# Performance work log

Measured on AMD Instinct MI355X. Metric: run time of the kernel, lower is better.

## Reference

```python
import jax, jax.numpy as jnp
import numpy as np

B, L, SIZE, HEADS, AH, NBR, KER, DEPTH = 64, 512, 128, 8, 16, 15, 16, 3
MAXD = 20.0
N = B * L
EDGE = KER + 3 + 9 + 1  # 29


def _normalize(v):
    return v / (jnp.linalg.norm(v, axis=-1, keepdims=True) + 1e-8)


def _frames(pos):
    # local orientation frame per residue from consecutive CA displacements
    u = _normalize(pos[1:] - pos[:-1])            # (N-1,3)
    up = jnp.concatenate([u[:1], u], axis=0)      # u_{i-1}
    un = jnp.concatenate([u, u[-1:]], axis=0)     # u_i
    b = _normalize(up - un)
    n = _normalize(jnp.cross(up, un))
    return jnp.stack([b, n, jnp.cross(b, n)], axis=-1)  # (N,3,3)


def setup_inputs() -> dict:
    key = jax.random.key(0)
    ks = jax.random.split(key, 16)
    g = lambda i, shape, s=1.0: jax.random.normal(ks[i], shape, jnp.float32) * s
    return {
        "tertiary": g(0, (N, 3, 3), 10.0),
        "sequence": g(1, (N, 20)),
        "subgraph_indices": jnp.arange(N, dtype=jnp.int32) // L,
        "knn_noise": g(2, (B, L, L)),
        "embed_w": g(3, (27, SIZE), 0.1), "embed_b": jnp.zeros((SIZE,), jnp.float32),
        "wq": g(4, (DEPTH, SIZE, HEADS * AH), 0.08),
        "wk": g(5, (DEPTH, SIZE + EDGE, HEADS * AH), 0.08),
        "wv": g(6, (DEPTH, SIZE + EDGE, HEADS * AH), 0.08),
        "wo": g(7, (DEPTH, HEADS * AH, SIZE), 0.08),
        "mlp_w1": g(8, (DEPTH, SIZE, SIZE), 0.08), "mlp_b1": jnp.zeros((DEPTH, SIZE), jnp.float32),
        "mlp_w2": g(9, (DEPTH, SIZE, SIZE), 0.08), "mlp_b2": jnp.zeros((DEPTH, SIZE), jnp.float32),
        "mlp_w3": g(10, (DEPTH, SIZE, SIZE), 0.08), "mlp_b3": jnp.zeros((DEPTH, SIZE), jnp.float32),
        "pool_w": g(11, (4, SIZE, SIZE, 3), 0.05), "pool_b": jnp.zeros((4, SIZE), jnp.float32),
        "energy_w": g(12, (SIZE, 1), 0.1), "energy_b": jnp.zeros((1,), jnp.float32),
    }


def _forward(tertiary, sequence, knn_noise, embed_w, embed_b, wq, wk, wv, wo,
             mlp_w1, mlp_b1, mlp_w2, mlp_b2, mlp_w3, mlp_b3,
             pool_w, pool_b, energy_w, energy_b):
    pos = tertiary[:, 1]                                   # (N,3) CA positions
    R = _frames(pos)                                       # (N,3,3)
    # ---- kNN per contiguous protein group with noisy distances ----
    pg = pos.reshape(B, L, 3)
    dist = jnp.linalg.norm(pg[:, :, None] - pg[:, None, :], axis=-1)  # (B,L,L)
    closeness = -dist + 3.0 * knn_noise
    idx = jax.lax.top_k(closeness, NBR)[1]                 # (B,L,NBR) local
    nbr = (idx + (jnp.arange(B) * L)[:, None, None]).reshape(N, NBR)
    # ---- RBF relative encoding (RelativeStructure.message) ----
    dvec = pos[nbr] - pos[:, None]                         # (N,NBR,3)
    d = jnp.linalg.norm(dvec, axis=-1)                     # (N,NBR)
    mu = jnp.linspace(0.0, MAXD, KER)
    sigma = MAXD / KER
    rbf = jnp.exp(-(((d[..., None] - mu) / sigma) ** 2))   # (N,NBR,KER)
    dirs = jnp.einsum('nrc,nkr->nkc', R, dvec / (d[..., None] + 1e-8))
    relrot = jnp.einsum('nrc,nkrd->nkcd', R, R[nbr]).reshape(N, NBR, 9)
    ind = jnp.arange(N, dtype=tertiary.dtype)
    relind = (ind[nbr] - ind[:, None])[..., None]
    edge = jnp.concatenate([rbf, dirs, relrot, relind], axis=-1)  # (N,NBR,EDGE)
    # ---- structured graph-attention encoder ----
    h = jnp.ones((N, 27), tertiary.dtype) @ embed_w + embed_b
    inv_sqrt = 1.0 / np.sqrt(AH).astype(np.float32)
    for l in range(DEPTH):
        q = (h @ wq[l]).reshape(N, HEADS, AH)
        kv = jnp.concatenate([h[nbr], edge], axis=-1)      # (N,NBR,SIZE+EDGE)
        k = (kv @ wk[l]).reshape(N, NBR, HEADS, AH)
        v = (kv @ wv[l]).reshape(N, NBR, HEADS, AH)
        logits = jnp.einsum('nhd,nkhd->nhk', q, k) * inv_sqrt
        a = jax.nn.softmax(logits, axis=-1)
        o = jnp.einsum('nhk,nkhd->nhd', a, v).reshape(N, HEADS * AH) @ wo[l]
        h = h + o
        m = jax.nn.relu(h @ mlp_w1[l] + mlp_b1[l])
        m = jax.nn.relu(m @ mlp_w2[l] + mlp_b2[l])
        h = h + m @ mlp_w3[l] + mlp_b3[l]
    # ---- scatter-pad pool: residual conv + maxpool(2), x4, then length-sum ----
    x = h.reshape(B, L, SIZE).transpose(0, 2, 1)           # (B,SIZE,L)
    for i in range(4):
        y = jax.lax.conv_general_dilated(
            x, pool_w[i], (1,), ((1, 1),),
            dimension_numbers=('NCH', 'OIH', 'NCH')) + pool_b[i][None, :, None]
        x = x + jax.nn.leaky_relu(y, 0.01)
        Lc = x.shape[-1]
        x = x.reshape(B, SIZE, Lc // 2, 2).max(axis=-1)
    pooled = x.sum(axis=-1)                                # (B,SIZE)
    return pooled @ energy_w + energy_b                    # (B,1)


def reference(tertiary, sequence, subgraph_indices, knn_noise, embed_w, embed_b,
              wq, wk, wv, wo, mlp_w1, mlp_b1, mlp_w2, mlp_b2, mlp_w3, mlp_b3,
              pool_w, pool_b, energy_w, energy_b):
    # subgraph_indices encodes contiguous equal-size groups (arange // L)
    return _forward(tertiary, sequence, knn_noise, embed_w, embed_b, wq, wk, wv, wo,
                    mlp_w1, mlp_b1, mlp_w2, mlp_b2, mlp_w3, mlp_b3,
                    pool_w, pool_b, energy_w, energy_b)
```

## Files before the change

kernel.cpp:

```cpp
#include <hip/hip_runtime.h>
#include <math.h>

#define N_TOT 32768
#define NNBR 15
#define APW 8
#define ELP 36
#define ETP 20
#define PLP 20

typedef __attribute__((ext_vector_type(8))) _Float16 f16x8;
typedef __attribute__((ext_vector_type(2))) _Float16 f16x2;
typedef __attribute__((ext_vector_type(4))) float f32x4;

#define CBAR() __asm__ volatile("" ::: "memory")

__device__ __forceinline__ _Float16 f2h(float x) { return (_Float16)x; }

__global__ __launch_bounds__(256) void k_frames(const float* __restrict__ tert,
                                                float* __restrict__ pos,
                                                float* __restrict__ R) {
  int n = blockIdx.x * 256 + threadIdx.x;
  if (n >= N_TOT) return;
  float px = tert[n * 9 + 3], py = tert[n * 9 + 4], pz = tert[n * 9 + 5];
  pos[n * 3 + 0] = px; pos[n * 3 + 1] = py; pos[n * 3 + 2] = pz;

  int i0 = (n > 0) ? (n - 1) : 0;
  int i1 = (n < N_TOT - 1) ? n : (N_TOT - 2);

  float ax = tert[(i0 + 1) * 9 + 3] - tert[i0 * 9 + 3];
  float ay = tert[(i0 + 1) * 9 + 4] - tert[i0 * 9 + 4];
  float az = tert[(i0 + 1) * 9 + 5] - tert[i0 * 9 + 5];
  float il = 1.f / (sqrtf(ax * ax + ay * ay + az * az) + 1e-8f);
  float ux = ax * il, uy = ay * il, uz = az * il;

  float cx = tert[(i1 + 1) * 9 + 3] - tert[i1 * 9 + 3];
  float cy = tert[(i1 + 1) * 9 + 4] - tert[i1 * 9 + 4];
  float cz = tert[(i1 + 1) * 9 + 5] - tert[i1 * 9 + 5];
  il = 1.f / (sqrtf(cx * cx + cy * cy + cz * cz) + 1e-8f);
  float vx = cx * il, vy = cy * il, vz = cz * il;

  float bx = ux - vx, by = uy - vy, bz = uz - vz;
  il = 1.f / (sqrtf(bx * bx + by * by + bz * bz) + 1e-8f);
  bx *= il; by *= il; bz *= il;

  float nx = uy * vz - uz * vy;
  float ny = uz * vx - ux * vz;
  float nz = ux * vy - uy * vx;
  il = 1.f / (sqrtf(nx * nx + ny * ny + nz * nz) + 1e-8f);
  nx *= il; ny *= il; nz *= il;

  float ex = by * nz - bz * ny;
  float ey = bz * nx - bx * nz;
  float ez = bx * ny - by * nx;

  float* Rn = R + (size_t)n * 9;
  Rn[0] = bx; Rn[1] = nx; Rn[2] = ex;
  Rn[3] = by; Rn[4] = ny; Rn[5] = ey;
  Rn[6] = bz; Rn[7] = nz; Rn[8] = ez;
}

template <int CTRL>
__device__ __forceinline__ unsigned long long dpp_max_u64(unsigned long long x) {
  unsigned lo = (unsigned)__builtin_amdgcn_update_dpp(
      0, (int)(unsigned)x, CTRL, 0xf, 0xf, true);
  unsigned hi = (unsigned)__builtin_amdgcn_update_dpp(
      0, (int)(unsigned)(x >> 32), CTRL, 0xf, 0xf, true);
  unsigned long long y = ((unsigned long long)hi << 32) | lo;
  return y > x ? y : x;
}

__global__ __launch_bounds__(256) void k_knn(const float* __restrict__ pos,
                                             const float* __restrict__ noise,
                                             int* __restrict__ nbr) {
  int wave = threadIdx.x >> 6, lane = threadIdx.x & 63;
  int row = blockIdx.x * 4 + wave;
  int b = row >> 9;
  float pix = pos[row * 3 + 0], piy = pos[row * 3 + 1], piz = pos[row * 3 + 2];
  const float* nrow = noise + (size_t)row * 512;
  const float* pb = pos + (size_t)b * 512 * 3;
  unsigned long long key[8];
#pragma unroll
  for (int jj = 0; jj < 8; jj++) {
    int j = lane + jj * 64;
    float dx = pb[j * 3 + 0] - pix;
    float dy = pb[j * 3 + 1] - piy;
    float dz = pb[j * 3 + 2] - piz;
    float c = -sqrtf(dx * dx + dy * dy + dz * dz) + 3.f * nrow[j];
    unsigned u = __float_as_uint(c);
    unsigned s = u ^ (unsigned)(((int)u >> 31) | (int)0x80000000);
    key[jj] = ((unsigned long long)s << 9) | (unsigned)(511 - j);
  }
  unsigned long long best = key[0];
#pragma unroll
  for (int jj = 1; jj < 8; jj++) best = key[jj] > best ? key[jj] : best;
  int jmine = 0;
#pragma unroll 1
  for (int it = 0; it < NNBR; it++) {
    unsigned long long r = best;
    r = dpp_max_u64<0x111>(r);
    r = dpp_max_u64<0x112>(r);
    r = dpp_max_u64<0x114>(r);
    r = dpp_max_u64<0x118>(r);
    r = dpp_max_u64<0x142>(r);
    r = dpp_max_u64<0x143>(r);
    unsigned glo = (unsigned)__builtin_amdgcn_readlane((int)(unsigned)r, 63);
    unsigned ghi = (unsigned)__builtin_amdgcn_readlane((int)(unsigned)(r >> 32), 63);
    unsigned long long g = ((unsigned long long)ghi << 32) | glo;
    int j = 511 - (int)(g & 511ull);
    if (lane == it) jmine = j;
    if ((j & 63) == lane) {
      int slot = j >> 6;
#pragma unroll
      for (int jj = 0; jj < 8; jj++) if (slot == jj) key[jj] = 0ull;
      best = key[0];
#pragma unroll
      for (int jj = 1; jj < 8; jj++) best = key[jj] > best ? key[jj] : best;
    }
  }
  if (lane < NNBR) nbr[(size_t)row * NNBR + lane] = b * 512 + jmine;
}

__global__ __launch_bounds__(256) void k_edge(const float* __restrict__ pos,
                                              const float* __restrict__ R,
                                              const int* __restrict__ nbr,
                                              _Float16* __restrict__ edge) {
  int idx = blockIdx.x * 256 + threadIdx.x;
  if (idx >= N_TOT * NNBR) return;
  int n = idx / NNBR;
  int m = nbr[idx];
  float dx = pos[m * 3 + 0] - pos[n * 3 + 0];
  float dy = pos[m * 3 + 1] - pos[n * 3 + 1];
  float dz = pos[m * 3 + 2] - pos[n * 3 + 2];
  float d = sqrtf(dx * dx + dy * dy + dz * dz);
  _Float16 eb[32];
#pragma unroll
  for (int j = 0; j < 16; j++) {
    float mu = (20.f / 15.f) * (float)j;
    float t = (d - mu) * 0.8f;
    eb[j] = f2h(__expf(-t * t));
  }
  float inv = 1.f / (d + 1e-8f);
  float ux = dx * inv, uy = dy * inv, uz = dz * inv;
  float Rn[9], Rm[9];
#pragma unroll
  for (int j = 0; j < 9; j++) { Rn[j] = R[(size_t)n * 9 + j]; Rm[j] = R[(size_t)m * 9 + j]; }
#pragma unroll
  for (int cc = 0; cc < 3; cc++)
    eb[16 + cc] = f2h(Rn[0 * 3 + cc] * ux + Rn[1 * 3 + cc] * uy + Rn[2 * 3 + cc] * uz);
#pragma unroll
  for (int cc = 0; cc < 3; cc++)
#pragma unroll
    for (int dd = 0; dd < 3; dd++)
      eb[19 + cc * 3 + dd] = f2h(Rn[0 * 3 + cc] * Rm[0 * 3 + dd] +
                                 Rn[1 * 3 + cc] * Rm[1 * 3 + dd] +
                                 Rn[2 * 3 + cc] * Rm[2 * 3 + dd]);
  eb[28] = f2h((float)(m - n));
  eb[29] = (_Float16)0.f; eb[30] = (_Float16)0.f; eb[31] = (_Float16)0.f;
  _Float16* e = edge + (size_t)idx * 32;
#pragma unroll
  for (int v = 0; v < 4; v++)
    *(uint4*)(e + v * 8) = *(const uint4*)(&eb[v * 8]);
}

__global__ __launch_bounds__(256) void k_prep_all(
    const float* __restrict__ wq, const float* __restrict__ wk,
    const float* __restrict__ wv, const float* __restrict__ wo,
    const float* __restrict__ w1, const float* __restrict__ w2,
    const float* __restrict__ w3, _Float16* __restrict__ wbt,
    _Float16* __restrict__ wqk, _Float16* __restrict__ wpe,
    const float* __restrict__ pw, _Float16* __restrict__ wct,
    const float* __restrict__ ew, const float* __restrict__ ebias,
    _Float16* __restrict__ h) {
  __shared__ float hv[128];
  int bb = blockIdx.x, tid = threadIdx.x;
  if (bb < 1344) {
    int idx = bb * 256 + tid;
    int l = idx / (7 * 16384);
    int r = idx % (7 * 16384);
    int w = r / 16384;
    int e = r % 16384;
    int k = e >> 7, n = e & 127;
    float val;
    switch (w) {
      case 0: val = wq[(size_t)l * 16384 + e]; break;
      case 1: val = wk[(size_t)l * 157 * 128 + e]; break;
      case 2: val = wv[(size_t)l * 157 * 128 + e]; break;
      case 3: val = wo[(size_t)l * 16384 + e]; break;
      case 4: val = w1[(size_t)l * 16384 + e]; break;
      case 5: val = w2[(size_t)l * 16384 + e]; break;
      default: val = w3[(size_t)l * 16384 + e]; break;
    }
    wbt[(size_t)(l * 7 + w) * 16384 + n * 128 + k] = f2h(val);
  } else if (bb < 1728) {
    int idx = (bb - 1344) * 256 + tid;
    int l = idx / 32768;
    int r = idx % 32768;
    int blk = r >> 14;
    int jp = (r >> 7) & 127;
    int c = r & 127;
    int j = blk * 128 + jp;
    int hh = j >> 5, e = j & 31;
    float val = 0.f;
    if (e < 29) {
      const float* wqp = wq + (size_t)l * 16384 + (size_t)c * 128 + hh * 16;
      const float* wkp = wk + (size_t)l * 157 * 128 + (size_t)(128 + e) * 128 + hh * 16;
      float s = 0.f;
#pragma unroll
      for (int d = 0; d < 16; d++) s = fmaf(wqp[d], wkp[d], s);
      val = 0.25f * s;
    }
    wqk[(size_t)idx] = f2h(val);
  } else if (bb < 2112) {
    int idx = (bb - 1728) * 256 + tid;
    int l = idx / 32768;
    int r = idx % 32768;
    int blk = r >> 14;
    int cout = (r >> 7) & 127;
    int jp = r & 127;
    int j = blk * 128 + jp;
    float val = 0.f;
    if (j < 232) {
      int e = j >> 3, hh = j & 7;
      const float* wvp = wv + (size_t)l * 157 * 128 + (size_t)(128 + e) * 128 + hh * 16;
      const float* wop = wo + (size_t)l * 16384 + (size_t)(hh * 16) * 128 + cout;
#pragma unroll
      for (int d = 0; d < 16; d++) val = fmaf(wvp[d], wop[d * 128], val);
    }
    wpe[(size_t)idx] = f2h(val);
  } else if (bb < 2880) {
    int idx = (bb - 2112) * 256 + tid;
    int kt = idx % 3;
    int rest = idx / 3;
    int i = rest % 128; rest /= 128;
    int oo = rest % 128;
    int s = rest / 128;
    wc_store:
    wct[(((size_t)s * 3 + kt) * 128 + oo) * 128 + i] = f2h(pw[idx]);
  } else {
    int vb = bb - 2880;
    if (tid < 128) {
      float s = ebias[tid];
#pragma unroll
      for (int i = 0; i < 27; i++) s += ew[i * 128 + tid];
      hv[tid] = s;
    }
    __syncthreads();
    size_t total = (size_t)N_TOT * 128;
    for (size_t j = (size_t)vb * 256 + tid; j < total; j += (size_t)512 * 256)
      h[j] = f2h(hv[j & 127]);
  }
}

__device__ __forceinline__ void stage_w(const _Float16* __restrict__ W, _Float16* Ws, int tid) {
  for (int j = tid; j < 2048; j += 256) {
    int row = j >> 4, seg = (j & 15) * 8;
    *(uint4*)&Ws[row * 136 + seg] = *(const uint4*)(W + (size_t)row * 128 + seg);
  }
}
__device__ __forceinline__ void stage_x(const _Float16* __restrict__ src, _Float16* X,
                                        int tid, int rowstride) {
  for (int j = tid; j < 1024; j += 256) {
    int row = j >> 4, seg = (j & 15) * 8;
    *(uint4*)&X[row * 136 + seg] = *(const uint4*)(src + (size_t)row * rowstride + seg);
  }
}
template <bool RESET>
__device__ __forceinline__ void gemm_tile_t(const _Float16* X, const _Float16* Ws,
                                            int wrow, int l16, int quad, f32x4 acc[8]) {
  if (RESET) {
#pragma unroll
    for (int t = 0; t < 8; t++) acc[t] = (f32x4){0.f, 0.f, 0.f, 0.f};
  }
#pragma unroll
  for (int kk = 0; kk < 4; kk++) {
    f16x8 a = *(const f16x8*)&X[(wrow + l16) * 136 + kk * 32 + quad * 8];
#pragma unroll
    for (int t = 0; t < 8; t++) {
      f16x8 b = *(const f16x8*)&Ws[(t * 16 + l16) * 136 + kk * 32 + quad * 8];
      acc[t] = __builtin_amdgcn_mfma_f32_16x16x32_f16(a, b, acc[t], 0, 0, 0);
    }
  }
}

__global__ __launch_bounds__(256) void k_qkv(const _Float16* __restrict__ A,
                                             const _Float16* __restrict__ Wqt,
                                             const _Float16* __restrict__ Wkt,
                                             const _Float16* __restrict__ Wvt,
                                             const _Float16* __restrict__ Wqk0,
                                             const _Float16* __restrict__ Wqk1,
                                             _Float16* __restrict__ q, _Float16* __restrict__ hk,
                                             _Float16* __restrict__ hv, _Float16* __restrict__ qkw) {
  __shared__ _Float16 X[64 * 136];
  __shared__ _Float16 Ws[128 * 136];
  int tid = threadIdx.x, r0 = blockIdx.x * 64;
  int lane = tid & 63, quad = lane >> 4, l16 = lane & 15, wrow = (tid >> 6) * 16;
  stage_x(A + (size_t)r0 * 128, X, tid, 128);
  const _Float16* wts[5] = {Wqt, Wkt, Wvt, Wqk0, Wqk1};
  f32x4 acc[8];
  for (int w = 0; w < 5; w++) {
    __syncthreads();
    stage_w(wts[w], Ws, tid);
    __syncthreads();
    gemm_tile_t<true>(X, Ws, wrow, l16, quad, acc);
#pragma unroll
    for (int t = 0; t < 8; t++) {
      int col = t * 16 + l16;
#pragma unroll
      for (int r = 0; r < 4; r++) {
        float v = acc[t][r];
        int rowg = r0 + wrow + quad * 4 + r;
        if (w < 3) {
          _Float16* C = (w == 0) ? q : (w == 1) ? hk : hv;
          C[(size_t)rowg * 128 + col] = f2h(v);
        } else {
          qkw[(size_t)rowg * 256 + (w - 3) * 128 + col] = f2h(v);
        }
      }
    }
  }
}

__global__ __launch_bounds__(256) void k_post(const _Float16* __restrict__ o,
                                              const _Float16* __restrict__ pe_g,
                                              _Float16* __restrict__ h,
                                              const _Float16* __restrict__ Wot,
                                              const _Float16* __restrict__ Wpe0,
                                              const _Float16* __restrict__ Wpe1,
                                              const _Float16* __restrict__ W1t, const float* __restrict__ B1,
                                              const _Float16* __restrict__ W2t, const float* __restrict__ B2,
                                              const _Float16* __restrict__ W3t, const float* __restrict__ B3,
                                              const _Float16* __restrict__ Wqt,
                                              const _Float16* __restrict__ Wkt,
                                              const _Float16* __restrict__ Wvt,
                                              const _Float16* __restrict__ Wqk0,
                                              const _Float16* __restrict__ Wqk1,
                                              _Float16* __restrict__ qo, _Float16* __restrict__ hko,
                                              _Float16* __restrict__ hvo, _Float16* __restrict__ qkwo,
                                              int do_qkv) {
  __shared__ _Float16 X[64 * 136];
  __shared__ _Float16 Ws[128 * 136];
  int tid = threadIdx.x, r0 = blockIdx.x * 64;
  int lane = tid & 63, quad = lane >> 4, l16 = lane & 15, wrow = (tid >> 6) * 16;
  f32x4 acc[8], hres[8];
  stage_x(o + (size_t)r0 * 128, X, tid, 128);
  stage_w(Wot, Ws, tid);
  __syncthreads();
  gemm_tile_t<true>(X, Ws, wrow, l16, quad, acc);
  const _Float16* wpes[2] = {Wpe0, Wpe1};
#pragma unroll 1
  for (int blk = 0; blk < 2; blk++) {
    __syncthreads();
    stage_x(pe_g + (size_t)r0 * 256 + blk * 128, X, tid, 256);
    stage_w(wpes[blk], Ws, tid);
    __syncthreads();
    gemm_tile_t<false>(X, Ws, wrow, l16, quad, acc);
  }
#pragma unroll
  for (int t = 0; t < 8; t++) {
    int col = t * 16 + l16;
#pragma unroll
    for (int r = 0; r < 4; r++)
      hres[t][r] = acc[t][r] + (float)h[(size_t)(r0 + wrow + quad * 4 + r) * 128 + col];
  }
  __syncthreads();
#pragma unroll
  for (int t = 0; t < 8; t++) {
    int col = t * 16 + l16;
#pragma unroll
    for (int r = 0; r < 4; r++)
      X[(wrow + quad * 4 + r) * 136 + col] = f2h(hres[t][r]);
  }
  stage_w(W1t, Ws, tid);
  __syncthreads();
  gemm_tile_t<true>(X, Ws, wrow, l16, quad, acc);
  __syncthreads();
#pragma unroll
  for (int t = 0; t < 8; t++) {
    int col = t * 16 + l16; float bv = B1[col];
#pragma unroll
    for (int r = 0; r < 4; r++)
      X[(wrow + quad * 4 + r) * 136 + col] = f2h(fmaxf(acc[t][r] + bv, 0.f));
  }
  stage_w(W2t, Ws, tid);
  __syncthreads();
  gemm_tile_t<true>(X, Ws, wrow, l16, quad, acc);
  __syncthreads();
#pragma unroll
  for (int t = 0; t < 8; t++) {
    int col = t * 16 + l16; float bv = B2[col];
#pragma unroll
    for (int r = 0; r < 4; r++)
      X[(wrow + quad * 4 + r) * 136 + col] = f2h(fmaxf(acc[t][r] + bv, 0.f));
  }
  stage_w(W3t, Ws, tid);
  __syncthreads();
  gemm_tile_t<true>(X, Ws, wrow, l16, quad, acc);
  __syncthreads();
#pragma unroll
  for (int t = 0; t < 8; t++) {
    int col = t * 16 + l16; float bv = B3[col];
#pragma unroll
    for (int r = 0; r < 4; r++) {
      float v = hres[t][r] + acc[t][r] + bv;
      h[(size_t)(r0 + wrow + quad * 4 + r) * 128 + col] = f2h(v);
      if (do_qkv) X[(wrow + quad * 4 + r) * 136 + col] = f2h(v);
    }
  }
  if (!do_qkv) return;
  const _Float16* wts[5] = {Wqt, Wkt, Wvt, Wqk0, Wqk1};
  for (int w = 0; w < 5; w++) {
    __syncthreads();
    stage_w(wts[w], Ws, tid);
    __syncthreads();
    gemm_tile_t<true>(X, Ws, wrow, l16, quad, acc);
#pragma unroll
    for (int t = 0; t < 8; t++) {
      int col = t * 16 + l16;
#pragma unroll
      for (int r = 0; r < 4; r++) {
        float v = acc[t][r];
        int rowg = r0 + wrow + quad * 4 + r;
        if (w < 3) {
          _Float16* C = (w == 0) ? qo : (w == 1) ? hko : hvo;
          C[(size_t)rowg * 128 + col] = f2h(v);
        } else {
          qkwo[(size_t)rowg * 256 + (w - 3) * 128 + col] = f2h(v);
        }
      }
    }
  }
}

__global__ __launch_bounds__(256) void k_attn(const _Float16* __restrict__ q,
                                              const _Float16* __restrict__ hk,
                                              const _Float16* __restrict__ hv,
                                              const int* __restrict__ nbr,
                                              const _Float16* __restrict__ edge,
                                              const _Float16* __restrict__ qkw,
                                              _Float16* __restrict__ o,
                                              _Float16* __restrict__ pe_g) {
  __shared__ float elL[4][15 * ELP];
  __shared__ float etL[4][32 * ETP];
  __shared__ float plL[4][8 * PLP];
  __shared__ int nbL[4][16];
  int tid = threadIdx.x, wave = tid >> 6, lane = tid & 63;
  float* el = elL[wave]; float* et = etL[wave]; float* pl = plL[wave];
  int* nbl = nbL[wave];
  int h8 = lane & 7, k2 = lane >> 3, c2 = lane * 2, h5 = lane >> 3;
  int kst = lane >> 2, gst = lane & 3;
  if (lane < 32) et[lane * ETP + 15] = 0.f;
  int n0 = (blockIdx.x * 4 + wave) * APW;
#pragma unroll 1
  for (int ni = 0; ni < APW; ni++) {
    int n = n0 + ni;
    if (lane < 60) {
      f16x8 ev = *(const f16x8*)(edge + ((size_t)n * 15 + kst) * 32 + gst * 8);
      float e0 = (float)ev[0], e1 = (float)ev[1], e2 = (float)ev[2], e3 = (float)ev[3];
      float e4 = (float)ev[4], e5 = (float)ev[5], e6 = (float)ev[6], e7 = (float)ev[7];
      *(f32x4*)&el[kst * ELP + gst * 8]     = (f32x4){e0, e1, e2, e3};
      *(f32x4*)&el[kst * ELP + gst * 8 + 4] = (f32x4){e4, e5, e6, e7};
      int ebs = gst * 8;
      et[(ebs + 0) * ETP + kst] = e0; et[(ebs + 1) * ETP + kst] = e1;
      et[(ebs + 2) * ETP + kst] = e2; et[(ebs + 3) * ETP + kst] = e3;
      et[(ebs + 4) * ETP + kst] = e4; et[(ebs + 5) * ETP + kst] = e5;
      et[(ebs + 6) * ETP + kst] = e6; et[(ebs + 7) * ETP + kst] = e7;
    }
    if (lane < 15) nbl[lane] = nbr[(size_t)n * NNBR + lane];
    const _Float16* qs = qkw + (size_t)n * 256 + h8 * 32;
    f16x8 w0 = *(const f16x8*)qs, w1 = *(const f16x8*)(qs + 8);
    f16x8 w2 = *(const f16x8*)(qs + 16), w3 = *(const f16x8*)(qs + 24);
    float qw[32];
#pragma unroll
    for (int d = 0; d < 8; d++) {
      qw[d] = (float)w0[d]; qw[8 + d] = (float)w1[d];
      qw[16 + d] = (float)w2[d]; qw[24 + d] = (float)w3[d];
    }
    const _Float16* qp = q + (size_t)n * 128 + h8 * 16;
    f16x8 qa = *(const f16x8*)qp, qb = *(const f16x8*)(qp + 8);
    float q16[16];
#pragma unroll
    for (int d = 0; d < 8; d++) { q16[d] = (float)qa[d]; q16[8 + d] = (float)qb[d]; }
    CBAR();
#pragma unroll
    for (int p = 0; p < 2; p++) {
      int k = k2 + p * 8;
      if (k < 15) {
        int m = nbl[k];
        const _Float16* hkp = hk + (size_t)m * 128 + h8 * 16;
        f16x8 ha = *(const f16x8*)hkp, hb = *(const f16x8*)(hkp + 8);
        float dot = 0.f;
#pragma unroll
        for (int d = 0; d < 8; d++) dot = fmaf(q16[d], (float)ha[d], dot);
#pragma unroll
        for (int d = 0; d < 8; d++) dot = fmaf(q16[8 + d], (float)hb[d], dot);
        float ep = 0.f;
#pragma unroll
        for (int c = 0; c < 8; c++) {
          f32x4 e4 = *(const f32x4*)&el[k * ELP + c * 4];
          ep = fmaf(e4[0], qw[c * 4 + 0], ep);
          ep = fmaf(e4[1], qw[c * 4 + 1], ep);
          ep = fmaf(e4[2], qw[c * 4 + 2], ep);
          ep = fmaf(e4[3], qw[c * 4 + 3], ep);
        }
        pl[h8 * PLP + k] = fmaf(0.25f, dot, ep);
      } else {
        pl[h8 * PLP + 15] = -1e30f;
      }
    }
    CBAR();
    if (lane < 8) {
      float v[16];
      *(f32x4*)&v[0]  = *(const f32x4*)&pl[lane * PLP + 0];
      *(f32x4*)&v[4]  = *(const f32x4*)&pl[lane * PLP + 4];
      *(f32x4*)&v[8]  = *(const f32x4*)&pl[lane * PLP + 8];
      *(f32x4*)&v[12] = *(const f32x4*)&pl[lane * PLP + 12];
      float mx = v[0];
#pragma unroll
      for (int i = 1; i < 15; i++) mx = fmaxf(mx, v[i]);
      float s = 0.f;
#pragma unroll
      for (int i = 0; i < 16; i++) { v[i] = __expf(v[i] - mx); s += v[i]; }
      float inv = 1.f / s;
#pragma unroll
      for (int i = 0; i < 16; i++) v[i] *= inv;
      *(f32x4*)&pl[lane * PLP + 0]  = *(const f32x4*)&v[0];
      *(f32x4*)&pl[lane * PLP + 4]  = *(const f32x4*)&v[4];
      *(f32x4*)&pl[lane * PLP + 8]  = *(const f32x4*)&v[8];
      *(f32x4*)&pl[lane * PLP + 12] = *(const f32x4*)&v[12];
    }
    CBAR();
    _Float16* peo = pe_g + (size_t)n * 256;
#pragma unroll
    for (int p = 0; p < 4; p++) {
      int j = p * 64 + lane;
      float s = 0.f;
      if (j < 232) {
        int e = j >> 3, hh = j & 7;
        f32x4 p0 = *(const f32x4*)&pl[hh * PLP + 0];
        f32x4 p1 = *(const f32x4*)&pl[hh * PLP + 4];
        f32x4 p2 = *(const f32x4*)&pl[hh * PLP + 8];
        f32x4 p3 = *(const f32x4*)&pl[hh * PLP + 12];
        f32x4 t0 = *(const f32x4*)&et[e * ETP + 0];
        f32x4 t1 = *(const f32x4*)&et[e * ETP + 4];
        f32x4 t2 = *(const f32x4*)&et[e * ETP + 8];
        f32x4 t3 = *(const f32x4*)&et[e * ETP + 12];
        s = p0[0]*t0[0] + p0[1]*t0[1] + p0[2]*t0[2] + p0[3]*t0[3]
          + p1[0]*t1[0] + p1[1]*t1[1] + p1[2]*t1[2] + p1[3]*t1[3]
          + p2[0]*t2[0] + p2[1]*t2[1] + p2[2]*t2[2] + p2[3]*t2[3]
          + p3[0]*t3[0] + p3[1]*t3[1] + p3[2]*t3[2] + p3[3]*t3[3];
      }
      peo[j] = f2h(s);
    }
    float pk[16];
    *(f32x4*)&pk[0]  = *(const f32x4*)&pl[h5 * PLP + 0];
    *(f32x4*)&pk[4]  = *(const f32x4*)&pl[h5 * PLP + 4];
    *(f32x4*)&pk[8]  = *(const f32x4*)&pl[h5 * PLP + 8];
    *(f32x4*)&pk[12] = *(const f32x4*)&pl[h5 * PLP + 12];
    float ox = 0.f, oy = 0.f;
#pragma unroll
    for (int k = 0; k < 15; k++) {
      int m = nbl[k];
      f16x2 hh = *(const f16x2*)(hv + (size_t)m * 128 + c2);
      ox = fmaf(pk[k], (float)hh[0], ox);
      oy = fmaf(pk[k], (float)hh[1], oy);
    }
    *(f16x2*)(o + (size_t)n * 128 + c2) = (f16x2){f2h(ox), f2h(oy)};
    CBAR();
  }
}

__global__ __launch_bounds__(256) void k_convpool_m(const _Float16* __restrict__ x,
                                                    const _Float16* __restrict__ Wc,
                                                    const float* __restrict__ bias,
                                                    _Float16* __restrict__ outp, int Tin) {
  __shared__ _Float16 Xs[66 * 136];
  __shared__ _Float16 Ws[128 * 136];
  int tid = threadIdx.x;
  int b = blockIdx.y;
  int t0 = blockIdx.x * 64;
  for (int j = tid; j < 66 * 16; j += 256) {
    int row = j >> 4, seg = (j & 15) * 8;
    int t = t0 - 1 + row;
    uint4 v = {0u, 0u, 0u, 0u};
    if (t >= 0 && t < Tin) v = *(const uint4*)(x + ((size_t)b * Tin + t) * 128 + seg);
    *(uint4*)&Xs[row * 136 + seg] = v;
  }
  int lane = tid & 63, quad = lane >> 4, l16 = lane & 15, wrow = (tid >> 6) * 16;
  f32x4 acc[8];
#pragma unroll
  for (int t = 0; t < 8; t++) acc[t] = (f32x4){0.f, 0.f, 0.f, 0.f};
  for (int kt = 0; kt < 3; kt++) {
    __syncthreads();
    stage_w(Wc + (size_t)kt * 16384, Ws, tid);
    __syncthreads();
#pragma unroll
    for (int kk = 0; kk < 4; kk++) {
      f16x8 a = *(const f16x8*)&Xs[(wrow + l16 + kt) * 136 + kk * 32 + quad * 8];
#pragma unroll
      for (int t = 0; t < 8; t++) {
        f16x8 bfr = *(const f16x8*)&Ws[(t * 16 + l16) * 136 + kk * 32 + quad * 8];
        acc[t] = __builtin_amdgcn_mfma_f32_16x16x32_f16(a, bfr, acc[t], 0, 0, 0);
      }
    }
  }
  int Tout = Tin >> 1;
#pragma unroll
  for (int t = 0; t < 8; t++) {
    int col = t * 16 + l16;
    float bv = bias[col];
#pragma unroll
    for (int rp = 0; rp < 2; rp++) {
      int rl0 = wrow + quad * 4 + rp * 2;
      float y0 = acc[t][rp * 2] + bv;
      float y1 = acc[t][rp * 2 + 1] + bv;
      float z0 = (float)Xs[(rl0 + 1) * 136 + col] + (y0 >= 0.f ? y0 : 0.01f * y0);
      float z1 = (float)Xs[(rl0 + 2) * 136 + col] + (y1 >= 0.f ? y1 : 0.01f * y1);
      outp[((size_t)b * Tout + ((t0 + rl0) >> 1)) * 128 + col] = f2h(fmaxf(z0, z1));
    }
  }
}

__global__ __launch_bounds__(128) void k_final(const _Float16* __restrict__ x,
                                               const float* __restrict__ ew,
                                               const float* __restrict__ ebb,
                                               float* __restrict__ outp) {
  int b = blockIdx.x, cc = threadIdx.x;
  float s = 0.f;
#pragma unroll
  for (int t = 0; t < 32; t++) s += (float)x[((size_t)b * 32 + t) * 128 + cc];
  float v = s * ew[cc];
#pragma unroll
  for (int m = 1; m < 64; m <<= 1) v += __shfl_xor(v, m);
  __shared__ float red[2];
  if ((cc & 63) == 0) red[cc >> 6] = v;
  __syncthreads();
  if (cc == 0) outp[b] = red[0] + red[1] + ebb[0];
}

extern "C" void kernel_launch(void* const* d_in, const int* in_sizes, int n_in,
                              void* d_out, int out_size, void* d_ws, size_t ws_size,
                              hipStream_t stream) {
  (void)in_sizes; (void)n_in; (void)out_size; (void)ws_size;
  const float* tert    = (const float*)d_in[0];
  const float* noise   = (const float*)d_in[3];
  const float* embed_w = (const float*)d_in[4];
  const float* embed_b = (const float*)d_in[5];
  const float* wq = (const float*)d_in[6];
  const float* wk = (const float*)d_in[7];
  const float* wv = (const float*)d_in[8];
  const float* wo = (const float*)d_in[9];
  const float* w1 = (const float*)d_in[10];
  const float* b1 = (const float*)d_in[11];
  const float* w2 = (const float*)d_in[12];
  const float* b2 = (const float*)d_in[13];
  const float* w3 = (const float*)d_in[14];
  const float* b3 = (const float*)d_in[15];
  const float* pw = (const float*)d_in[16];
  const float* pb = (const float*)d_in[17];
  const float* ew = (const float*)d_in[18];
  const float* eb = (const float*)d_in[19];
  float* outp = (float*)d_out;

  char* W = (char*)d_ws;
  float* pos  = (float*)W;        W += 393216;
  float* R    = (float*)W;        W += 1179648;
  int*   nbr  = (int*)W;          W += 1966080;
  _Float16* edge = (_Float16*)W;  W += 31457280;
  _Float16* h    = (_Float16*)W;  W += 8388608;
  _Float16* q    = (_Float16*)W;  W += 8388608;
  _Float16* hk   = (_Float16*)W;  W += 8388608;
  _Float16* hv   = (_Float16*)W;  W += 8388608;
  _Float16* o    = (_Float16*)W;  W += 8388608;
  _Float16* qkw_g = (_Float16*)W; W += 16777216;
  _Float16* pe_g  = (_Float16*)W; W += 16777216;
  _Float16* xa   = (_Float16*)W;  W += 4194304;
  _Float16* xb   = (_Float16*)W;  W += 2097152;
  _Float16* wbt  = (_Float16*)W;  W += 688128;
  _Float16* wqk  = (_Float16*)W;  W += 196608;
  _Float16* wpe  = (_Float16*)W;  W += 196608;
  _Float16* wct  = (_Float16*)W;  W += 393216;

  k_frames<<<128, 256, 0, stream>>>(tert, pos, R);
  k_knn<<<8192, 256, 0, stream>>>(pos, noise, nbr);
  k_edge<<<1920, 256, 0, stream>>>(pos, R, nbr, edge);
  k_prep_all<<<3392, 256, 0, stream>>>(wq, wk, wv, wo, w1, w2, w3, wbt,
                                       wqk, wpe, pw, wct, embed_w, embed_b, h);

  const _Float16* wt[3][7];
  for (int l = 0; l < 3; l++)
    for (int w = 0; w < 7; w++) wt[l][w] = wbt + (size_t)(l * 7 + w) * 16384;
  const _Float16* wqk_l[3][2];
  const _Float16* wpe_l[3][2];
  for (int l = 0; l < 3; l++)
    for (int bk = 0; bk < 2; bk++) {
      wqk_l[l][bk] = wqk + (size_t)(l * 2 + bk) * 16384;
      wpe_l[l][bk] = wpe + (size_t)(l * 2 + bk) * 16384;
    }

  k_qkv<<<512, 256, 0, stream>>>(h, wt[0][0], wt[0][1], wt[0][2],
                                 wqk_l[0][0], wqk_l[0][1], q, hk, hv, qkw_g);
  for (int l = 0; l < 3; l++) {
    k_attn<<<1024, 256, 0, stream>>>(q, hk, hv, nbr, edge, qkw_g, o, pe_g);
    int nl = l + 1;
    int do_qkv = (nl < 3) ? 1 : 0;
    k_post<<<512, 256, 0, stream>>>(o, pe_g, h, wt[l][3],
                                    wpe_l[l][0], wpe_l[l][1],
                                    wt[l][4], b1 + l * 128,
                                    wt[l][5], b2 + l * 128,
                                    wt[l][6], b3 + l * 128,
                                    do_qkv ? wt[nl][0] : nullptr,
                                    do_qkv ? wt[nl][1] : nullptr,
                                    do_qkv ? wt[nl][2] : nullptr,
                                    do_qkv ? wqk_l[nl][0] : nullptr,
                                    do_qkv ? wqk_l[nl][1] : nullptr,
                                    q, hk, hv, qkw_g, do_qkv);
  }

  k_convpool_m<<<dim3(8, 64), 256, 0, stream>>>(h,  wct + 0 * 49152, pb + 0,   xa, 512);
  k_convpool_m<<<dim3(4, 64), 256, 0, stream>>>(xa, wct + 1 * 49152, pb + 128, xb, 256);
  k_convpool_m<<<dim3(2, 64), 256, 0, stream>>>(xb, wct + 2 * 49152, pb + 256, xa, 128);
  k_convpool_m<<<dim3(1, 64), 256, 0, stream>>>(xa, wct + 3 * 49152, pb + 384, xb, 64);
  k_final<<<64, 128, 0, stream>>>(xb, ew, eb, outp);
}
```

Before: 541.4 us.

## Fuse frames, kNN and weight prep into one launch with half-wave top-3 kNN

Merges the frames, kNN and weight-prep kernels into one launch, with each block range doing one role, which removes two launch boundaries and lets the independent work overlap. The kNN now handles two rows per wave, 32 lanes per row. Positions are staged in shared memory, read directly from tert. Each lane keeps a top-3 list instead of all 8 keys, and rescans its candidates under a threshold only when its list runs out. This cuts registers and the reduction depth, at the cost of a possible divergent recompute path and a more complex kernel.

```diff
diff --git a/kernel.cpp b/kernel.cpp
--- a/kernel.cpp
+++ b/kernel.cpp
@@ -8,6 +8,10 @@
 #define ETP 20
 #define PLP 20
 
+#define KNB 4096
+#define FRB 128
+#define PRB 3392
+
 typedef __attribute__((ext_vector_type(8))) _Float16 f16x8;
 typedef __attribute__((ext_vector_type(2))) _Float16 f16x2;
 typedef __attribute__((ext_vector_type(4))) float f32x4;
@@ -15,49 +19,6 @@
 #define CBAR() __asm__ volatile("" ::: "memory")
 
 __device__ __forceinline__ _Float16 f2h(float x) { return (_Float16)x; }
-
-__global__ __launch_bounds__(256) void k_frames(const float* __restrict__ tert,
-                                                float* __restrict__ pos,
-                                                float* __restrict__ R) {
-  int n = blockIdx.x * 256 + threadIdx.x;
-  if (n >= N_TOT) return;
-  float px = tert[n * 9 + 3], py = tert[n * 9 + 4], pz = tert[n * 9 + 5];
-  pos[n * 3 + 0] = px; pos[n * 3 + 1] = py; pos[n * 3 + 2] = pz;
-
-  int i0 = (n > 0) ? (n - 1) : 0;
-  int i1 = (n < N_TOT - 1) ? n : (N_TOT - 2);
-
-  float ax = tert[(i0 + 1) * 9 + 3] - tert[i0 * 9 + 3];
-  float ay = tert[(i0 + 1) * 9 + 4] - tert[i0 * 9 + 4];
-  float az = tert[(i0 + 1) * 9 + 5] - tert[i0 * 9 + 5];
-  float il = 1.f / (sqrtf(ax * ax + ay * ay + az * az) + 1e-8f);
-  float ux = ax * il, uy = ay * il, uz = az * il;
-
-  float cx = tert[(i1 + 1) * 9 + 3] - tert[i1 * 9 + 3];
-  float cy = tert[(i1 + 1) * 9 + 4] - tert[i1 * 9 + 4];
-  float cz = tert[(i1 + 1) * 9 + 5] - tert[i1 * 9 + 5];
-  il = 1.f / (sqrtf(cx * cx + cy * cy + cz * cz) + 1e-8f);
-  float vx = cx * il, vy = cy * il, vz = cz * il;
-
-  float bx = ux - vx, by = uy - vy, bz = uz - vz;
-  il = 1.f / (sqrtf(bx * bx + by * by + bz * bz) + 1e-8f);
-  bx *= il; by *= il; bz *= il;
-
-  float nx = uy * vz - uz * vy;
-  float ny = uz * vx - ux * vz;
-  float nz = ux * vy - uy * vx;
-  il = 1.f / (sqrtf(nx * nx + ny * ny + nz * nz) + 1e-8f);
-  nx *= il; ny *= il; nz *= il;
-
-  float ex = by * nz - bz * ny;
-  float ey = bz * nx - bx * nz;
-  float ez = bx * ny - by * nx;
-
-  float* Rn = R + (size_t)n * 9;
-  Rn[0] = bx; Rn[1] = nx; Rn[2] = ex;
-  Rn[3] = by; Rn[4] = ny; Rn[5] = ey;
-  Rn[6] = bz; Rn[7] = nz; Rn[8] = ez;
-}
 
 template <int CTRL>
 __device__ __forceinline__ unsigned long long dpp_max_u64(unsigned long long x) {
@@ -69,55 +30,213 @@
   return y > x ? y : x;
 }
 
-__global__ __launch_bounds__(256) void k_knn(const float* __restrict__ pos,
-                                             const float* __restrict__ noise,
-                                             int* __restrict__ nbr) {
-  int wave = threadIdx.x >> 6, lane = threadIdx.x & 63;
-  int row = blockIdx.x * 4 + wave;
-  int b = row >> 9;
-  float pix = pos[row * 3 + 0], piy = pos[row * 3 + 1], piz = pos[row * 3 + 2];
-  const float* nrow = noise + (size_t)row * 512;
-  const float* pb = pos + (size_t)b * 512 * 3;
-  unsigned long long key[8];
-#pragma unroll
-  for (int jj = 0; jj < 8; jj++) {
-    int j = lane + jj * 64;
-    float dx = pb[j * 3 + 0] - pix;
-    float dy = pb[j * 3 + 1] - piy;
-    float dz = pb[j * 3 + 2] - piz;
-    float c = -sqrtf(dx * dx + dy * dy + dz * dz) + 3.f * nrow[j];
-    unsigned u = __float_as_uint(c);
-    unsigned s = u ^ (unsigned)(((int)u >> 31) | (int)0x80000000);
-    key[jj] = ((unsigned long long)s << 9) | (unsigned)(511 - j);
-  }
-  unsigned long long best = key[0];
-#pragma unroll
-  for (int jj = 1; jj < 8; jj++) best = key[jj] > best ? key[jj] : best;
-  int jmine = 0;
+__device__ __forceinline__ void ins3(unsigned long long k,
+                                     unsigned long long& m1,
+                                     unsigned long long& m2,
+                                     unsigned long long& m3) {
+  unsigned long long t1 = k > m1 ? k : m1;
+  unsigned long long r1 = k > m1 ? m1 : k;
+  unsigned long long t2 = r1 > m2 ? r1 : m2;
+  unsigned long long r2 = r1 > m2 ? m2 : r1;
+  unsigned long long t3 = r2 > m3 ? r2 : m3;
+  m1 = t1; m2 = t2; m3 = t3;
+}
+
+__global__ __launch_bounds__(256) void k_pre(
+    const float* __restrict__ tert, const float* __restrict__ noise,
+    int* __restrict__ nbr, float* __restrict__ pos, float* __restrict__ R,
+    const float* __restrict__ wq, const float* __restrict__ wk,
+    const float* __restrict__ wv, const float* __restrict__ wo,
+    const float* __restrict__ w1, const float* __restrict__ w2,
+    const float* __restrict__ w3, _Float16* __restrict__ wbt,
+    _Float16* __restrict__ wqk, _Float16* __restrict__ wpe,
+    const float* __restrict__ pw, _Float16* __restrict__ wct,
+    const float* __restrict__ ew, const float* __restrict__ ebias,
+    _Float16* __restrict__ h) {
+  __shared__ float posL[512 * 3];
+  __shared__ float hvS[128];
+  int bb = blockIdx.x, tid = threadIdx.x;
+  if (bb < KNB) {
+    int b = bb >> 6;
+    int n0 = b << 9;
+    for (int i = tid; i < 1536; i += 256) {
+      int r = i / 3, c = i - r * 3;
+      posL[i] = tert[(size_t)(n0 + r) * 9 + 3 + c];
+    }
+    __syncthreads();
+    int wave = tid >> 6, lane = tid & 63;
+    int l = lane & 31;
+    int rloc = (bb & 63) * 8 + wave * 2 + (lane >> 5);
+    int row = n0 + rloc;
+    const float* nrow = noise + (size_t)row * 512;
+    float pix = posL[rloc * 3 + 0];
+    float piy = posL[rloc * 3 + 1];
+    float piz = posL[rloc * 3 + 2];
+    unsigned long long m1 = 0ull, m2 = 0ull, m3 = 0ull;
+#pragma unroll
+    for (int jj = 0; jj < 16; jj++) {
+      int j = l + jj * 32;
+      float dx = posL[j * 3 + 0] - pix;
+      float dy = posL[j * 3 + 1] - piy;
+      float dz = posL[j * 3 + 2] - piz;
+      float c = -sqrtf(dx * dx + dy * dy + dz * dz) + 3.f * nrow[j];
+      unsigned u = __float_as_uint(c);
+      unsigned s = u ^ (unsigned)(((int)u >> 31) | (int)0x80000000);
+      unsigned long long k = ((unsigned long long)s << 9) | (unsigned)(511 - j);
+      ins3(k, m1, m2, m3);
+    }
+    int jmine = 0;
 #pragma unroll 1
-  for (int it = 0; it < NNBR; it++) {
-    unsigned long long r = best;
-    r = dpp_max_u64<0x111>(r);
-    r = dpp_max_u64<0x112>(r);
-    r = dpp_max_u64<0x114>(r);
-    r = dpp_max_u64<0x118>(r);
-    r = dpp_max_u64<0x142>(r);
-    r = dpp_max_u64<0x143>(r);
-    unsigned glo = (unsigned)__builtin_amdgcn_readlane((int)(unsigned)r, 63);
-    unsigned ghi = (unsigned)__builtin_amdgcn_readlane((int)(unsigned)(r >> 32), 63);
-    unsigned long long g = ((unsigned long long)ghi << 32) | glo;
-    int j = 511 - (int)(g & 511ull);
-    if (lane == it) jmine = j;
-    if ((j & 63) == lane) {
-      int slot = j >> 6;
-#pragma unroll
-      for (int jj = 0; jj < 8; jj++) if (slot == jj) key[jj] = 0ull;
-      best = key[0];
-#pragma unroll
-      for (int jj = 1; jj < 8; jj++) best = key[jj] > best ? key[jj] : best;
-    }
-  }
-  if (lane < NNBR) nbr[(size_t)row * NNBR + lane] = b * 512 + jmine;
+    for (int it = 0; it < NNBR; it++) {
+      unsigned long long r = m1;
+      r = dpp_max_u64<0x111>(r);
+      r = dpp_max_u64<0x112>(r);
+      r = dpp_max_u64<0x114>(r);
+      r = dpp_max_u64<0x118>(r);
+      r = dpp_max_u64<0x142>(r);
+      unsigned gloA = (unsigned)__builtin_amdgcn_readlane((int)(unsigned)r, 31);
+      unsigned ghiA = (unsigned)__builtin_amdgcn_readlane((int)(unsigned)(r >> 32), 31);
+      unsigned gloB = (unsigned)__builtin_amdgcn_readlane((int)(unsigned)r, 63);
+      unsigned ghiB = (unsigned)__builtin_amdgcn_readlane((int)(unsigned)(r >> 32), 63);
+      int jA = 511 - (int)(gloA & 511u);
+      int jB = 511 - (int)(gloB & 511u);
+      int j = (lane & 32) ? jB : jA;
+      if (l == it) jmine = j;
+      bool win = ((j & 31) == l);
+      if (win) { m1 = m2; m2 = m3; m3 = 0ull; }
+      if (__any((int)(win && m1 == 0ull))) {
+        if (win && m1 == 0ull) {
+          unsigned long long gthr = (lane & 32)
+              ? (((unsigned long long)ghiB << 32) | gloB)
+              : (((unsigned long long)ghiA << 32) | gloA);
+          unsigned long long a1 = 0ull, a2 = 0ull, a3 = 0ull;
+#pragma unroll 1
+          for (int jj = 0; jj < 16; jj++) {
+            int j2 = l + jj * 32;
+            float dx = posL[j2 * 3 + 0] - pix;
+            float dy = posL[j2 * 3 + 1] - piy;
+            float dz = posL[j2 * 3 + 2] - piz;
+            float c = -sqrtf(dx * dx + dy * dy + dz * dz) + 3.f * nrow[j2];
+            unsigned u = __float_as_uint(c);
+            unsigned s = u ^ (unsigned)(((int)u >> 31) | (int)0x80000000);
+            unsigned long long k = ((unsigned long long)s << 9) | (unsigned)(511 - j2);
+            if (k < gthr) ins3(k, a1, a2, a3);
+          }
+          m1 = a1; m2 = a2; m3 = a3;
+        }
+      }
+    }
+    if (l < NNBR) nbr[(size_t)row * NNBR + l] = n0 + jmine;
+  } else if (bb < KNB + FRB) {
+    int n = (bb - KNB) * 256 + tid;
+    if (n >= N_TOT) return;
+    float px = tert[n * 9 + 3], py = tert[n * 9 + 4], pz = tert[n * 9 + 5];
+    pos[n * 3 + 0] = px; pos[n * 3 + 1] = py; pos[n * 3 + 2] = pz;
+    int i0 = (n > 0) ? (n - 1) : 0;
+    int i1 = (n < N_TOT - 1) ? n : (N_TOT - 2);
+    float ax = tert[(i0 + 1) * 9 + 3] - tert[i0 * 9 + 3];
+    float ay = tert[(i0 + 1) * 9 + 4] - tert[i0 * 9 + 4];
+    float az = tert[(i0 + 1) * 9 + 5] - tert[i0 * 9 + 5];
+    float il = 1.f / (sqrtf(ax * ax + ay * ay + az * az) + 1e-8f);
+    float ux = ax * il, uy = ay * il, uz = az * il;
+    float cx = tert[(i1 + 1) * 9 + 3] - tert[i1 * 9 + 3];
+    float cy = tert[(i1 + 1) * 9 + 4] - tert[i1 * 9 + 4];
+    float cz = tert[(i1 + 1) * 9 + 5] - tert[i1 * 9 + 5];
+    il = 1.f / (sqrtf(cx * cx + cy * cy + cz * cz) + 1e-8f);
+    float vx = cx * il, vy = cy * il, vz = cz * il;
+    float bx = ux - vx, by = uy - vy, bz = uz - vz;
+    il = 1.f / (sqrtf(bx * bx + by * by + bz * bz) + 1e-8f);
+    bx *= il; by *= il; bz *= il;
+    float nx = uy * vz - uz * vy;
+    float ny = uz * vx - ux * vz;
+    float nz = ux * vy - uy * vx;
+    il = 1.f / (sqrtf(nx * nx + ny * ny + nz * nz) + 1e-8f);
+    nx *= il; ny *= il; nz *= il;
+    float ex = by * nz - bz * ny;
+    float ey = bz * nx - bx * nz;
+    float ez = bx * ny - by * nx;
+    float* Rn = R + (size_t)n * 9;
+    Rn[0] = bx; Rn[1] = nx; Rn[2] = ex;
+    Rn[3] = by; Rn[4] = ny; Rn[5] = ey;
+    Rn[6] = bz; Rn[7] = nz; Rn[8] = ez;
+  } else {
+    int pb2 = bb - (KNB + FRB);
+    if (pb2 < 1344) {
+      int idx = pb2 * 256 + tid;
+      int lL = idx / (7 * 16384);
+      int r = idx % (7 * 16384);
+      int w = r / 16384;
+      int e = r % 16384;
+      int k = e >> 7, n = e & 127;
+      float val;
+      switch (w) {
+        case 0: val = wq[(size_t)lL * 16384 + e]; break;
+        case 1: val = wk[(size_t)lL * 157 * 128 + e]; break;
+        case 2: val = wv[(size_t)lL * 157 * 128 + e]; break;
+        case 3: val = wo[(size_t)lL * 16384 + e]; break;
+        case 4: val = w1[(size_t)lL * 16384 + e]; break;
+        case 5: val = w2[(size_t)lL * 16384 + e]; break;
+        default: val = w3[(size_t)lL * 16384 + e]; break;
+      }
+      wbt[(size_t)(lL * 7 + w) * 16384 + n * 128 + k] = f2h(val);
+    } else if (pb2 < 1728) {
+      int idx = (pb2 - 1344) * 256 + tid;
+      int lL = idx / 32768;
+      int r = idx % 32768;
+      int blk = r >> 14;
+      int jp = (r >> 7) & 127;
+      int c = r & 127;
+      int j = blk * 128 + jp;
+      int hh = j >> 5, e = j & 31;
+      float val = 0.f;
+      if (e < 29) {
+        const float* wqp = wq + (size_t)lL * 16384 + (size_t)c * 128 + hh * 16;
+        const float* wkp = wk + (size_t)lL * 157 * 128 + (size_t)(128 + e) * 128 + hh * 16;
+        float s = 0.f;
+#pragma unroll
+        for (int d = 0; d < 16; d++) s = fmaf(wqp[d], wkp[d], s);
+        val = 0.25f * s;
+      }
+      wqk[(size_t)idx] = f2h(val);
+    } else if (pb2 < 2112) {
+      int idx = (pb2 - 1728) * 256 + tid;
+      int lL = idx / 32768;
+      int r = idx % 32768;
+      int blk = r >> 14;
+      int cout = (r >> 7) & 127;
+      int jp = r & 127;
+      int j = blk * 128 + jp;
+      float val = 0.f;
+      if (j < 232) {
+        int e = j >> 3, hh = j & 7;
+        const float* wvp = wv + (size_t)lL * 157 * 128 + (size_t)(128 + e) * 128 + hh * 16;
+        const float* wop = wo + (size_t)lL * 16384 + (size_t)(hh * 16) * 128 + cout;
+#pragma unroll
+        for (int d = 0; d < 16; d++) val = fmaf(wvp[d], wop[d * 128], val);
+      }
+      wpe[(size_t)idx] = f2h(val);
+    } else if (pb2 < 2880) {
+      int idx = (pb2 - 2112) * 256 + tid;
+      int kt = idx % 3;
+      int rest = idx / 3;
+      int i = rest % 128; rest /= 128;
+      int oo = rest % 128;
+      int s = rest / 128;
+      wct[(((size_t)s * 3 + kt) * 128 + oo) * 128 + i] = f2h(pw[idx]);
+    } else {
+      int vb = pb2 - 2880;
+      if (tid < 128) {
+        float s = ebias[tid];
+#pragma unroll
+        for (int i = 0; i < 27; i++) s += ew[i * 128 + tid];
+        hvS[tid] = s;
+      }
+      __syncthreads();
+      size_t total = (size_t)N_TOT * 128;
+      for (size_t j = (size_t)vb * 256 + tid; j < total; j += (size_t)512 * 256)
+        h[j] = f2h(hvS[j & 127]);
+    }
+  }
 }
 
 __global__ __launch_bounds__(256) void k_edge(const float* __restrict__ pos,
@@ -160,95 +279,6 @@
 #pragma unroll
   for (int v = 0; v < 4; v++)
     *(uint4*)(e + v * 8) = *(const uint4*)(&eb[v * 8]);
-}
-
-__global__ __launch_bounds__(256) void k_prep_all(
-    const float* __restrict__ wq, const float* __restrict__ wk,
-    const float* __restrict__ wv, const float* __restrict__ wo,
-    const float* __restrict__ w1, const float* __restrict__ w2,
-    const float* __restrict__ w3, _Float16* __restrict__ wbt,
-    _Float16* __restrict__ wqk, _Float16* __restrict__ wpe,
-    const float* __restrict__ pw, _Float16* __restrict__ wct,
-    const float* __restrict__ ew, const float* __restrict__ ebias,
-    _Float16* __restrict__ h) {
-  __shared__ float hv[128];
-  int bb = blockIdx.x, tid = threadIdx.x;
-  if (bb < 1344) {
-    int idx = bb * 256 + tid;
-    int l = idx / (7 * 16384);
-    int r = idx % (7 * 16384);
-    int w = r / 16384;
-    int e = r % 16384;
-    int k = e >> 7, n = e & 127;
-    float val;
-    switch (w) {
-      case 0: val = wq[(size_t)l * 16384 + e]; break;
-      case 1: val = wk[(size_t)l * 157 * 128 + e]; break;
-      case 2: val = wv[(size_t)l * 157 * 128 + e]; break;
-      case 3: val = wo[(size_t)l * 16384 + e]; break;
-      case 4: val = w1[(size_t)l * 16384 + e]; break;
-      case 5: val = w2[(size_t)l * 16384 + e]; break;
-      default: val = w3[(size_t)l * 16384 + e]; break;
-    }
-    wbt[(size_t)(l * 7 + w) * 16384 + n * 128 + k] = f2h(val);
-  } else if (bb < 1728) {
-    int idx = (bb - 1344) * 256 + tid;
-    int l = idx / 32768;
-    int r = idx % 32768;
-    int blk = r >> 14;
-    int jp = (r >> 7) & 127;
-    int c = r & 127;
-    int j = blk * 128 + jp;
-    int hh = j >> 5, e = j & 31;
-    float val = 0.f;
-    if (e < 29) {
-      const float* wqp = wq + (size_t)l * 16384 + (size_t)c * 128 + hh * 16;
-      const float* wkp = wk + (size_t)l * 157 * 128 + (size_t)(128 + e) * 128 + hh * 16;
-      float s = 0.f;
-#pragma unroll
-      for (int d = 0; d < 16; d++) s = fmaf(wqp[d], wkp[d], s);
-      val = 0.25f * s;
-    }
-    wqk[(size_t)idx] = f2h(val);
-  } else if (bb < 2112) {
-    int idx = (bb - 1728) * 256 + tid;
-    int l = idx / 32768;
-    int r = idx % 32768;
-    int blk = r >> 14;
-    int cout = (r >> 7) & 127;
-    int jp = r & 127;
-    int j = blk * 128 + jp;
-    float val = 0.f;
-    if (j < 232) {
-      int e = j >> 3, hh = j & 7;
-      const float* wvp = wv + (size_t)l * 157 * 128 + (size_t)(128 + e) * 128 + hh * 16;
-      const float* wop = wo + (size_t)l * 16384 + (size_t)(hh * 16) * 128 + cout;
-#pragma unroll
-      for (int d = 0; d < 16; d++) val = fmaf(wvp[d], wop[d * 128], val);
-    }
-    wpe[(size_t)idx] = f2h(val);
-  } else if (bb < 2880) {
-    int idx = (bb - 2112) * 256 + tid;
-    int kt = idx % 3;
-    int rest = idx / 3;
-    int i = rest % 128; rest /= 128;
-    int oo = rest % 128;
-    int s = rest / 128;
-    wc_store:
-    wct[(((size_t)s * 3 + kt) * 128 + oo) * 128 + i] = f2h(pw[idx]);
-  } else {
-    int vb = bb - 2880;
-    if (tid < 128) {
-      float s = ebias[tid];
-#pragma unroll
-      for (int i = 0; i < 27; i++) s += ew[i * 128 + tid];
-      hv[tid] = s;
-    }
-    __syncthreads();
-    size_t total = (size_t)N_TOT * 128;
-    for (size_t j = (size_t)vb * 256 + tid; j < total; j += (size_t)512 * 256)
-      h[j] = f2h(hv[j & 127]);
-  }
 }
 
 __device__ __forceinline__ void stage_w(const _Float16* __restrict__ W, _Float16* Ws, int tid) {
@@ -680,11 +710,10 @@
   _Float16* wpe  = (_Float16*)W;  W += 196608;
   _Float16* wct  = (_Float16*)W;  W += 393216;
 
-  k_frames<<<128, 256, 0, stream>>>(tert, pos, R);
-  k_knn<<<8192, 256, 0, stream>>>(pos, noise, nbr);
+  k_pre<<<KNB + FRB + PRB, 256, 0, stream>>>(tert, noise, nbr, pos, R,
+                                             wq, wk, wv, wo, w1, w2, w3, wbt,
+                                             wqk, wpe, pw, wct, embed_w, embed_b, h);
   k_edge<<<1920, 256, 0, stream>>>(pos, R, nbr, edge);
-  k_prep_all<<<3392, 256, 0, stream>>>(wq, wk, wv, wo, w1, w2, w3, wbt,
-                                       wqk, wpe, pw, wct, embed_w, embed_b, h);
 
   const _Float16* wt[3][7];
   for (int l = 0; l < 3; l++)
```

Result: faster. 514.6 us (-4.9%).
